# Kernel optimization log

Measured on AMD Instinct MI355X. Metric: run time of the kernel, lower is better.

Reference implementation:

```python
import jax, jax.numpy as jnp
import numpy as np
import math

NUM_HEADS = 16
HEAD_DIM = 32  # latent_dim // num_heads = 512 // 16


def rope(x, pos):
    # x: (B, H, S, Dh); half-split rotary embedding, theta=10000
    d = x.shape[-1] // 2
    inv_freq = 1.0 / (10000.0 ** (jnp.arange(d, dtype=jnp.float32) / d))
    ang = pos.astype(jnp.float32)[:, None] * inv_freq[None, :]  # (S, d)
    cos, sin = jnp.cos(ang), jnp.sin(ang)
    x1, x2 = x[..., :d], x[..., d:]
    return jnp.concatenate([x1 * cos - x2 * sin, x1 * sin + x2 * cos], axis=-1)


def setup_inputs() -> dict:
    key = jax.random.key(0)
    ks = jax.random.split(key, 16)
    B, L, KV_PREV = 1, 2048, 2048
    D, D_KV = 2048, 512
    s = lambda fan_in: 1.0 / math.sqrt(fan_in)
    return {
        "x": jax.random.normal(ks[0], (B, L, D), jnp.float32),
        "z_cache": jax.random.normal(ks[1], (B, KV_PREV, D_KV), jnp.float32),
        "valid_lens": jax.random.randint(ks[2], (B, L), 1, KV_PREV + L, jnp.int32),
        "W_latent": jax.random.normal(ks[3], (D, D_KV), jnp.float32) * s(D),
        "b_latent": jnp.zeros((D_KV,), jnp.float32),
        "W_q": jax.random.normal(ks[4], (D, NUM_HEADS * HEAD_DIM), jnp.float32) * s(D),
        "b_q": jnp.zeros((NUM_HEADS * HEAD_DIM,), jnp.float32),
        "W_k": jax.random.normal(ks[5], (D_KV, NUM_HEADS * HEAD_DIM), jnp.float32) * s(D_KV),
        "b_k": jnp.zeros((NUM_HEADS * HEAD_DIM,), jnp.float32),
        "W_v": jax.random.normal(ks[6], (D_KV, NUM_HEADS * HEAD_DIM), jnp.float32) * s(D_KV),
        "b_v": jnp.zeros((NUM_HEADS * HEAD_DIM,), jnp.float32),
        "W_o": jax.random.normal(ks[7], (NUM_HEADS * HEAD_DIM, D), jnp.float32) * s(NUM_HEADS * HEAD_DIM),
        "b_o": jnp.zeros((D,), jnp.float32),
    }


def reference(x, z_cache, valid_lens, W_latent, b_latent, W_q, b_q, W_k, b_k, W_v, b_v, W_o, b_o):
    B, L, D = x.shape
    H, Dh = NUM_HEADS, HEAD_DIM
    # latent projection + cache concat
    z_new = x @ W_latent + b_latent                      # (B, L, D_kv)
    z = jnp.concatenate([z_cache, z_new], axis=1)        # (B, KV, D_kv)
    KV = z.shape[1]
    q = (x @ W_q + b_q).reshape(B, L, H, Dh).transpose(0, 2, 1, 3)   # (B,H,L,Dh)
    k = (z @ W_k + b_k).reshape(B, KV, H, Dh).transpose(0, 2, 1, 3)  # (B,H,KV,Dh)
    v = (z @ W_v + b_v).reshape(B, KV, H, Dh).transpose(0, 2, 1, 3)  # (B,H,KV,Dh)
    q = rope(q, jnp.arange(L))
    k = rope(k, jnp.arange(KV))
    scores = jnp.einsum("bhqd,bhkd->bhqk", q, k) / math.sqrt(Dh)     # (B,H,L,KV)
    # faithful: unmasked softmax (returned as attn_weights), then re-masked softmax
    attn_weights = jax.nn.softmax(scores, axis=-1)
    invalid = jnp.arange(KV)[None, None, None, :] >= valid_lens[:, None, :, None]
    masked = jnp.where(invalid, jnp.float32(-10000.0), scores)
    masked_w = jax.nn.softmax(masked, axis=-1)
    heads = jnp.einsum("bhqk,bhkd->bhqd", masked_w, v)               # (B,H,L,Dh)
    heads = heads.transpose(0, 2, 1, 3).reshape(B, L, H * Dh)
    output = heads @ W_o + b_o                                       # (B, L, D)
    return (output, z, attn_weights, scores)
```

## Files before the change

### kernel.cpp

```cpp
#include <hip/hip_runtime.h>
#include <math.h>

#define L_Q     2048
#define KV_PREV 2048
#define KV_TOT  4096
#define DIM     2048
#define D_KV    512
#define NH      16
#define DH      32
#define HDh     512
#define KC      256

typedef short bf16x8 __attribute__((ext_vector_type(8)));
typedef short bf16x4 __attribute__((ext_vector_type(4)));
typedef float f32x4  __attribute__((ext_vector_type(4)));

__device__ inline short f2bf(float f) {
    unsigned u = __float_as_uint(f);
    u += 0x7fff + ((u >> 16) & 1);
    return (short)(u >> 16);
}

__device__ __constant__ double c_invfreq[16] = {
    1.0, 0.5623413251903491, 0.31622776601683794, 0.17782794100389228,
    0.1, 0.05623413251903491, 0.03162277660168379, 0.017782794100389228,
    0.01, 0.005623413251903491, 0.0031622776601683794, 0.0017782794100389228,
    0.001, 0.0005623413251903491, 0.00031622776601683794, 0.00017782794100389227,
};

__global__ void cvt_bf16(const float* __restrict__ in, short* __restrict__ out, int n8) {
    int i = blockIdx.x * blockDim.x + threadIdx.x;
    if (i >= n8) return;
    float4 a = reinterpret_cast<const float4*>(in)[2 * i];
    float4 b = reinterpret_cast<const float4*>(in)[2 * i + 1];
    union { short s[8]; int4 v; } u;
    u.s[0] = f2bf(a.x); u.s[1] = f2bf(a.y); u.s[2] = f2bf(a.z); u.s[3] = f2bf(a.w);
    u.s[4] = f2bf(b.x); u.s[5] = f2bf(b.y); u.s[6] = f2bf(b.z); u.s[7] = f2bf(b.w);
    reinterpret_cast<int4*>(out)[i] = u.v;
}

__global__ void cvt_copy(const float* __restrict__ src, float* __restrict__ dst,
                         short* __restrict__ dbf, int n8) {
    int i = blockIdx.x * blockDim.x + threadIdx.x;
    if (i >= n8) return;
    float4 a = reinterpret_cast<const float4*>(src)[2 * i];
    float4 b = reinterpret_cast<const float4*>(src)[2 * i + 1];
    reinterpret_cast<float4*>(dst)[2 * i]     = a;
    reinterpret_cast<float4*>(dst)[2 * i + 1] = b;
    union { short s[8]; int4 v; } u;
    u.s[0] = f2bf(a.x); u.s[1] = f2bf(a.y); u.s[2] = f2bf(a.z); u.s[3] = f2bf(a.w);
    u.s[4] = f2bf(b.x); u.s[5] = f2bf(b.y); u.s[6] = f2bf(b.z); u.s[7] = f2bf(b.w);
    reinterpret_cast<int4*>(dbf)[i] = u.v;
}

__global__ __launch_bounds__(256) void tr_cvt(const float* __restrict__ in,
        short* __restrict__ out, int K, int N) {
    __shared__ float tile[32][33];
    int k0 = blockIdx.x * 32, n0 = blockIdx.y * 32;
    int c = threadIdx.x & 31, r0 = threadIdx.x >> 5;
    for (int r = r0; r < 32; r += 8)
        tile[r][c] = in[(size_t)(k0 + r) * N + n0 + c];
    __syncthreads();
    for (int r = r0; r < 32; r += 8)
        out[(size_t)(n0 + r) * K + k0 + c] = f2bf(tile[c][r]);
}

__global__ __launch_bounds__(256) void vt_cvt(const short* __restrict__ v, short* __restrict__ vt) {
    __shared__ short tile[64][34];
    int h = blockIdx.y, kv0 = blockIdx.x * 64;
    int c = threadIdx.x & 31, r0 = threadIdx.x >> 5;
    for (int r = r0; r < 64; r += 8)
        tile[r][c] = v[(size_t)(kv0 + r) * HDh + h * DH + c];
    __syncthreads();
    int l = threadIdx.x & 63, wv = threadIdx.x >> 6;
    for (int d = wv; d < 32; d += 4)
        vt[((size_t)h * DH + d) * KV_TOT + kv0 + l] = tile[l][d];
}

__global__ __launch_bounds__(256) void gemm_bf16(const short* __restrict__ A,
        const short* __restrict__ Bt, const float* __restrict__ bias,
        float* __restrict__ C, short* __restrict__ Cbf, int rope,
        int M, int N, int K)
{
    int t = threadIdx.x, w = t >> 6, l = t & 63, lr = l & 15, lg = l >> 4;
    int m0 = blockIdx.y * 64 + w * 16;
    int n0 = blockIdx.x * 64;
    f32x4 acc[4] = {{0,0,0,0},{0,0,0,0},{0,0,0,0},{0,0,0,0}};
    const short* ap  = A  + (size_t)(m0 + lr) * K + lg * 8;
    const short* bp0 = Bt + (size_t)(n0 + lr) * K + lg * 8;
    #pragma unroll 2
    for (int k0 = 0; k0 < K; k0 += 32) {
        bf16x8 a = *reinterpret_cast<const bf16x8*>(ap + k0);
        #pragma unroll
        for (int j = 0; j < 4; ++j) {
            bf16x8 b = *reinterpret_cast<const bf16x8*>(bp0 + (size_t)j * 16 * K + k0);
            acc[j] = __builtin_amdgcn_mfma_f32_16x16x32_bf16(a, b, acc[j], 0, 0, 0);
        }
    }
    float bs[4];
    #pragma unroll
    for (int j = 0; j < 4; ++j) bs[j] = bias[n0 + j * 16 + lr];

    if (rope) {
        #pragma unroll
        for (int r = 0; r < 4; ++r) {
            int m = m0 + lg * 4 + r;
            float ang = (float)((double)m * c_invfreq[lr]);
            float cs = cosf(ang), sn = sinf(ang);
            size_t rb = (size_t)m * N + n0 + lr;
            float a1 = acc[0][r] + bs[0], a2 = acc[1][r] + bs[1];
            Cbf[rb]      = f2bf(a1 * cs - a2 * sn);
            Cbf[rb + 16] = f2bf(a1 * sn + a2 * cs);
            float b1 = acc[2][r] + bs[2], b2 = acc[3][r] + bs[3];
            Cbf[rb + 32] = f2bf(b1 * cs - b2 * sn);
            Cbf[rb + 48] = f2bf(b1 * sn + b2 * cs);
        }
        return;
    }
    #pragma unroll
    for (int j = 0; j < 4; ++j) {
        int n = n0 + j * 16 + lr;
        #pragma unroll
        for (int r = 0; r < 4; ++r) {
            float v = acc[j][r] + bs[j];
            size_t idx = (size_t)(m0 + lg * 4 + r) * N + n;
            if (C)   C[idx] = v;
            if (Cbf) Cbf[idx] = f2bf(v);
        }
    }
}

__global__ __launch_bounds__(256) void scores_stats(const short* __restrict__ q,
        const short* __restrict__ kmat, const int* __restrict__ vlens,
        float* __restrict__ scores, float* __restrict__ isu_o, float* __restrict__ is2_o)
{
    __shared__ float Sl[4][16][KC + 4];
    int t = threadIdx.x, w = t >> 6, l = t & 63, lr = l & 15, lg = l >> 4;
    int h = blockIdx.y;
    int qrow = blockIdx.x * 64 + w * 16;
    int myq = qrow + lr;
    bf16x8 bQ = *reinterpret_cast<const bf16x8*>(q + (size_t)myq * HDh + h * DH + lg * 8);
    int vl = vlens[myq];
    const short* kp = kmat + h * DH + lg * 8;
    const float sc = 0.17677669529663687f;
    float su = 0.f, s2 = 0.f;
    const int kb = lg * 4;

    bf16x8 a0 = *reinterpret_cast<const bf16x8*>(kp + (size_t)lr * HDh);
    bf16x8 a1 = *reinterpret_cast<const bf16x8*>(kp + (size_t)(16 + lr) * HDh);
    for (int c = 0; c < KV_TOT / KC; ++c) {
        #pragma unroll
        for (int kt = 0; kt < KC / 32; ++kt) {
            int k0 = c * KC + kt * 32;
            int kn = (k0 + 32) & (KV_TOT - 1);
            bf16x8 a0n = *reinterpret_cast<const bf16x8*>(kp + (size_t)(kn + lr) * HDh);
            bf16x8 a1n = *reinterpret_cast<const bf16x8*>(kp + (size_t)(kn + 16 + lr) * HDh);
            f32x4 z4 = {0.f, 0.f, 0.f, 0.f};
            f32x4 s0 = __builtin_amdgcn_mfma_f32_16x16x32_bf16(a0, bQ, z4, 0, 0, 0);
            f32x4 s1 = __builtin_amdgcn_mfma_f32_16x16x32_bf16(a1, bQ, z4, 0, 0, 0);
            f32x4 o0, o1;
            #pragma unroll
            for (int r = 0; r < 4; ++r) { o0[r] = s0[r] * sc; o1[r] = s1[r] * sc; }
            *reinterpret_cast<f32x4*>(&Sl[w][lr][kt * 32 + kb])      = o0;
            *reinterpret_cast<f32x4*>(&Sl[w][lr][kt * 32 + 16 + kb]) = o1;
            #pragma unroll
            for (int r = 0; r < 4; ++r) {
                float e0 = __expf(o0[r]), e1 = __expf(o1[r]);
                su += e0 + e1;
                if (k0 + kb + r < vl)      s2 += e0;
                if (k0 + 16 + kb + r < vl) s2 += e1;
            }
            a0 = a0n; a1 = a1n;
        }
        #pragma unroll
        for (int r = 0; r < 16; ++r) {
            f32x4 v = *reinterpret_cast<const f32x4*>(&Sl[w][r][l * 4]);
            float* dst = scores + ((size_t)h * L_Q + qrow + r) * KV_TOT + c * KC + l * 4;
            __builtin_nontemporal_store(v, reinterpret_cast<f32x4*>(dst));
        }
    }
    su += __shfl_xor(su, 16, 64); su += __shfl_xor(su, 32, 64);
    s2 += __shfl_xor(s2, 16, 64); s2 += __shfl_xor(s2, 32, 64);
    if (lg == 0) {
        size_t idx = (size_t)h * L_Q + myq;
        isu_o[idx] = 1.f / su;
        is2_o[idx] = 1.f / s2;
    }
}

__global__ __launch_bounds__(256) void attn_pv(const short* __restrict__ q,
        const short* __restrict__ kmat, const int* __restrict__ vlens,
        const float* __restrict__ isu_i, const float* __restrict__ is2_i,
        const short* __restrict__ Vt,
        float* __restrict__ attn, short* __restrict__ heads_bf)
{
    __shared__ float Al[4][16][KC + 4];
    __shared__ short Plds[4][16][72];
    int t = threadIdx.x, w = t >> 6, l = t & 63, lr = l & 15, lg = l >> 4;
    int h = blockIdx.y;
    int qrow = blockIdx.x * 64 + w * 16;
    int myq = qrow + lr;
    bf16x8 bQ = *reinterpret_cast<const bf16x8*>(q + (size_t)myq * HDh + h * DH + lg * 8);
    int vl = vlens[myq];
    size_t sidx = (size_t)h * L_Q + myq;
    float isu = isu_i[sidx], is2 = is2_i[sidx];
    const short* kp  = kmat + h * DH + lg * 8;
    const short* vp0 = Vt + ((size_t)h * DH + lr) * KV_TOT + lg * 8;
    const short* vp1 = vp0 + (size_t)16 * KV_TOT;
    const float sc = 0.17677669529663687f;
    short* prow = &Plds[w][lr][0];
    f32x4 h0 = {0,0,0,0}, h1 = {0,0,0,0};

    for (int c = 0; c < KV_TOT / KC; ++c) {
        #pragma unroll
        for (int g = 0; g < KC / 64; ++g) {
            #pragma unroll
            for (int kt = 0; kt < 4; ++kt) {
                int kk = c * KC + g * 64 + kt * 16;
                bf16x8 aK = *reinterpret_cast<const bf16x8*>(kp + (size_t)(kk + lr) * HDh);
                f32x4 z4 = {0.f, 0.f, 0.f, 0.f};
                f32x4 s = __builtin_amdgcn_mfma_f32_16x16x32_bf16(aK, bQ, z4, 0, 0, 0);
                f32x4 oa;
                bf16x4 pb;
                #pragma unroll
                for (int r = 0; r < 4; ++r) {
                    float e = __expf(s[r] * sc);
                    oa[r] = e * isu;
                    pb[r] = (kk + lg * 4 + r < vl) ? f2bf(e * is2) : (short)0;
                }
                *reinterpret_cast<f32x4*>(&Al[w][lr][g * 64 + kt * 16 + lg * 4]) = oa;
                *reinterpret_cast<bf16x4*>(prow + kt * 16 + lg * 4) = pb;
            }
            #pragma unroll
            for (int kbl = 0; kbl < 2; ++kbl) {
                int kv = c * KC + g * 64 + kbl * 32;
                bf16x8 pa = *reinterpret_cast<const bf16x8*>(prow + kbl * 32 + lg * 8);
                bf16x8 b0 = *reinterpret_cast<const bf16x8*>(vp0 + kv);
                bf16x8 b1 = *reinterpret_cast<const bf16x8*>(vp1 + kv);
                h0 = __builtin_amdgcn_mfma_f32_16x16x32_bf16(pa, b0, h0, 0, 0, 0);
                h1 = __builtin_amdgcn_mfma_f32_16x16x32_bf16(pa, b1, h1, 0, 0, 0);
            }
        }
        #pragma unroll
        for (int r = 0; r < 16; ++r) {
            f32x4 v = *reinterpret_cast<const f32x4*>(&Al[w][r][l * 4]);
            float* dst = attn + ((size_t)h * L_Q + qrow + r) * KV_TOT + c * KC + l * 4;
            __builtin_nontemporal_store(v, reinterpret_cast<f32x4*>(dst));
        }
    }
    #pragma unroll
    for (int r = 0; r < 4; ++r) {
        size_t ho = (size_t)(qrow + lg * 4 + r) * HDh + h * DH + lr;
        heads_bf[ho]      = f2bf(h0[r]);
        heads_bf[ho + 16] = f2bf(h1[r]);
    }
}

extern "C" void kernel_launch(void* const* d_in, const int* in_sizes, int n_in,
                              void* d_out, int out_size, void* d_ws, size_t ws_size,
                              hipStream_t stream) {
    const float* x       = (const float*)d_in[0];
    const float* z_cache = (const float*)d_in[1];
    const int*   vlens   = (const int*)  d_in[2];
    const float* W_lat   = (const float*)d_in[3];
    const float* b_lat   = (const float*)d_in[4];
    const float* W_q     = (const float*)d_in[5];
    const float* b_q     = (const float*)d_in[6];
    const float* W_k     = (const float*)d_in[7];
    const float* b_k     = (const float*)d_in[8];
    const float* W_v     = (const float*)d_in[9];
    const float* b_v     = (const float*)d_in[10];
    const float* W_o     = (const float*)d_in[11];
    const float* b_o     = (const float*)d_in[12];

    float* out        = (float*)d_out;
    float* out_output = out;
    float* out_z      = out_output + (size_t)L_Q * DIM;
    float* out_attn   = out_z + (size_t)KV_TOT * D_KV;
    float* out_scores = out_attn + (size_t)NH * L_Q * KV_TOT;

    float* wf     = (float*)d_ws;
    float* ws_isu = wf;
    float* ws_is2 = ws_isu + (size_t)NH * L_Q;
    short* wsb      = (short*)(ws_is2 + (size_t)NH * L_Q);
    short* x_bf     = wsb;
    short* z_bf     = x_bf + (size_t)L_Q * DIM;
    short* q_bf     = z_bf + (size_t)KV_TOT * D_KV;
    short* k_bf     = q_bf + (size_t)L_Q * HDh;
    short* v_bf     = k_bf + (size_t)KV_TOT * HDh;
    short* Vt       = v_bf + (size_t)KV_TOT * HDh;
    short* heads_bf = Vt + (size_t)NH * DH * KV_TOT;
    short* Wt_lat   = heads_bf + (size_t)L_Q * HDh;
    short* Wt_q     = Wt_lat + (size_t)D_KV * DIM;
    short* Wt_k     = Wt_q + (size_t)HDh * DIM;
    short* Wt_v     = Wt_k + (size_t)HDh * D_KV;
    short* Wt_o     = Wt_v + (size_t)HDh * D_KV;

    cvt_bf16<<<(L_Q * DIM / 8 + 255) / 256, 256, 0, stream>>>(x, x_bf, L_Q * DIM / 8);
    cvt_copy<<<(KV_PREV * D_KV / 8 + 255) / 256, 256, 0, stream>>>(
        z_cache, out_z, z_bf, KV_PREV * D_KV / 8);
    tr_cvt<<<dim3(DIM / 32, D_KV / 32), 256, 0, stream>>>(W_lat, Wt_lat, DIM, D_KV);
    tr_cvt<<<dim3(DIM / 32, HDh / 32), 256, 0, stream>>>(W_q, Wt_q, DIM, HDh);
    tr_cvt<<<dim3(D_KV / 32, HDh / 32), 256, 0, stream>>>(W_k, Wt_k, D_KV, HDh);
    tr_cvt<<<dim3(D_KV / 32, HDh / 32), 256, 0, stream>>>(W_v, Wt_v, D_KV, HDh);
    tr_cvt<<<dim3(HDh / 32, DIM / 32), 256, 0, stream>>>(W_o, Wt_o, HDh, DIM);

    gemm_bf16<<<dim3(D_KV / 64, L_Q / 64), 256, 0, stream>>>(
        x_bf, Wt_lat, b_lat, out_z + (size_t)KV_PREV * D_KV,
        z_bf + (size_t)KV_PREV * D_KV, 0, L_Q, D_KV, DIM);

    gemm_bf16<<<dim3(HDh / 64, L_Q / 64), 256, 0, stream>>>(
        x_bf, Wt_q, b_q, nullptr, q_bf, 1, L_Q, HDh, DIM);
    gemm_bf16<<<dim3(HDh / 64, KV_TOT / 64), 256, 0, stream>>>(
        z_bf, Wt_k, b_k, nullptr, k_bf, 1, KV_TOT, HDh, D_KV);
    gemm_bf16<<<dim3(HDh / 64, KV_TOT / 64), 256, 0, stream>>>(
        z_bf, Wt_v, b_v, nullptr, v_bf, 0, KV_TOT, HDh, D_KV);
    vt_cvt<<<dim3(KV_TOT / 64, NH), 256, 0, stream>>>(v_bf, Vt);

    scores_stats<<<dim3(L_Q / 64, NH), 256, 0, stream>>>(
        q_bf, k_bf, vlens, out_scores, ws_isu, ws_is2);

    attn_pv<<<dim3(L_Q / 64, NH), 256, 0, stream>>>(
        q_bf, k_bf, vlens, ws_isu, ws_is2, Vt, out_attn, heads_bf);

    gemm_bf16<<<dim3(DIM / 64, L_Q / 64), 256, 0, stream>>>(
        heads_bf, Wt_o, b_o, out_output, nullptr, 0, L_Q, DIM, HDh);
}
```

Baseline: 560.1 us.

## Prefetch whole K/V chunks into registers and shrink chunk size

New measurement: 586.1 us. 4.6% more time.

```diff
diff --git a/kernel.cpp b/kernel.cpp
--- a/kernel.cpp
+++ b/kernel.cpp
@@ -9,7 +9,7 @@
 #define NH      16
 #define DH      32
 #define HDh     512
-#define KC      256
+#define KC      128
 
 typedef short bf16x8 __attribute__((ext_vector_type(8)));
 typedef short bf16x4 __attribute__((ext_vector_type(4)));
@@ -146,38 +146,41 @@
     float su = 0.f, s2 = 0.f;
     const int kb = lg * 4;
 
-    bf16x8 a0 = *reinterpret_cast<const bf16x8*>(kp + (size_t)lr * HDh);
-    bf16x8 a1 = *reinterpret_cast<const bf16x8*>(kp + (size_t)(16 + lr) * HDh);
+    bf16x8 a[8], an[8];
+    #pragma unroll
+    for (int i = 0; i < 8; ++i)
+        a[i] = *reinterpret_cast<const bf16x8*>(kp + (size_t)(i * 16 + lr) * HDh);
+
+    #pragma unroll 2
     for (int c = 0; c < KV_TOT / KC; ++c) {
-        #pragma unroll
-        for (int kt = 0; kt < KC / 32; ++kt) {
-            int k0 = c * KC + kt * 32;
-            int kn = (k0 + 32) & (KV_TOT - 1);
-            bf16x8 a0n = *reinterpret_cast<const bf16x8*>(kp + (size_t)(kn + lr) * HDh);
-            bf16x8 a1n = *reinterpret_cast<const bf16x8*>(kp + (size_t)(kn + 16 + lr) * HDh);
+        int kbase = c * KC;
+        int knext = (kbase + KC) & (KV_TOT - 1);
+        #pragma unroll
+        for (int i = 0; i < 8; ++i)
+            an[i] = *reinterpret_cast<const bf16x8*>(kp + (size_t)(knext + i * 16 + lr) * HDh);
+        #pragma unroll
+        for (int i = 0; i < 8; ++i) {
             f32x4 z4 = {0.f, 0.f, 0.f, 0.f};
-            f32x4 s0 = __builtin_amdgcn_mfma_f32_16x16x32_bf16(a0, bQ, z4, 0, 0, 0);
-            f32x4 s1 = __builtin_amdgcn_mfma_f32_16x16x32_bf16(a1, bQ, z4, 0, 0, 0);
-            f32x4 o0, o1;
-            #pragma unroll
-            for (int r = 0; r < 4; ++r) { o0[r] = s0[r] * sc; o1[r] = s1[r] * sc; }
-            *reinterpret_cast<f32x4*>(&Sl[w][lr][kt * 32 + kb])      = o0;
-            *reinterpret_cast<f32x4*>(&Sl[w][lr][kt * 32 + 16 + kb]) = o1;
+            f32x4 s = __builtin_amdgcn_mfma_f32_16x16x32_bf16(a[i], bQ, z4, 0, 0, 0);
+            f32x4 o;
+            #pragma unroll
+            for (int r = 0; r < 4; ++r) o[r] = s[r] * sc;
+            *reinterpret_cast<f32x4*>(&Sl[w][lr][i * 16 + kb]) = o;
             #pragma unroll
             for (int r = 0; r < 4; ++r) {
-                float e0 = __expf(o0[r]), e1 = __expf(o1[r]);
-                su += e0 + e1;
-                if (k0 + kb + r < vl)      s2 += e0;
-                if (k0 + 16 + kb + r < vl) s2 += e1;
+                float e = __expf(o[r]);
+                su += e;
+                if (kbase + i * 16 + kb + r < vl) s2 += e;
             }
-            a0 = a0n; a1 = a1n;
         }
         #pragma unroll
         for (int r = 0; r < 16; ++r) {
-            f32x4 v = *reinterpret_cast<const f32x4*>(&Sl[w][r][l * 4]);
-            float* dst = scores + ((size_t)h * L_Q + qrow + r) * KV_TOT + c * KC + l * 4;
-            __builtin_nontemporal_store(v, reinterpret_cast<f32x4*>(dst));
-        }
+            float2 v = *reinterpret_cast<const float2*>(&Sl[w][r][l * 2]);
+            *reinterpret_cast<float2*>(
+                scores + ((size_t)h * L_Q + qrow + r) * KV_TOT + kbase + l * 2) = v;
+        }
+        #pragma unroll
+        for (int i = 0; i < 8; ++i) a[i] = an[i];
     }
     su += __shfl_xor(su, 16, 64); su += __shfl_xor(su, 32, 64);
     s2 += __shfl_xor(s2, 16, 64); s2 += __shfl_xor(s2, 32, 64);
@@ -208,45 +211,71 @@
     const short* vp0 = Vt + ((size_t)h * DH + lr) * KV_TOT + lg * 8;
     const short* vp1 = vp0 + (size_t)16 * KV_TOT;
     const float sc = 0.17677669529663687f;
+    const int kb = lg * 4;
     short* prow = &Plds[w][lr][0];
     f32x4 h0 = {0,0,0,0}, h1 = {0,0,0,0};
 
+    bf16x8 aK[8], aKn[8], vf[8], vfn[8];
+    #pragma unroll
+    for (int i = 0; i < 8; ++i)
+        aK[i] = *reinterpret_cast<const bf16x8*>(kp + (size_t)(i * 16 + lr) * HDh);
+    #pragma unroll
+    for (int g = 0; g < 2; ++g)
+        #pragma unroll
+        for (int kbl = 0; kbl < 2; ++kbl) {
+            vf[g * 4 + kbl * 2 + 0] = *reinterpret_cast<const bf16x8*>(vp0 + g * 64 + kbl * 32);
+            vf[g * 4 + kbl * 2 + 1] = *reinterpret_cast<const bf16x8*>(vp1 + g * 64 + kbl * 32);
+        }
+
+    #pragma unroll 2
     for (int c = 0; c < KV_TOT / KC; ++c) {
-        #pragma unroll
-        for (int g = 0; g < KC / 64; ++g) {
+        int kbase = c * KC;
+        int knext = (kbase + KC) & (KV_TOT - 1);
+        #pragma unroll
+        for (int i = 0; i < 8; ++i)
+            aKn[i] = *reinterpret_cast<const bf16x8*>(kp + (size_t)(knext + i * 16 + lr) * HDh);
+        #pragma unroll
+        for (int g = 0; g < 2; ++g)
+            #pragma unroll
+            for (int kbl = 0; kbl < 2; ++kbl) {
+                vfn[g * 4 + kbl * 2 + 0] =
+                    *reinterpret_cast<const bf16x8*>(vp0 + knext + g * 64 + kbl * 32);
+                vfn[g * 4 + kbl * 2 + 1] =
+                    *reinterpret_cast<const bf16x8*>(vp1 + knext + g * 64 + kbl * 32);
+            }
+        #pragma unroll
+        for (int g = 0; g < 2; ++g) {
             #pragma unroll
             for (int kt = 0; kt < 4; ++kt) {
-                int kk = c * KC + g * 64 + kt * 16;
-                bf16x8 aK = *reinterpret_cast<const bf16x8*>(kp + (size_t)(kk + lr) * HDh);
+                int i = g * 4 + kt;
                 f32x4 z4 = {0.f, 0.f, 0.f, 0.f};
-                f32x4 s = __builtin_amdgcn_mfma_f32_16x16x32_bf16(aK, bQ, z4, 0, 0, 0);
+                f32x4 s = __builtin_amdgcn_mfma_f32_16x16x32_bf16(aK[i], bQ, z4, 0, 0, 0);
                 f32x4 oa;
                 bf16x4 pb;
                 #pragma unroll
                 for (int r = 0; r < 4; ++r) {
                     float e = __expf(s[r] * sc);
                     oa[r] = e * isu;
-                    pb[r] = (kk + lg * 4 + r < vl) ? f2bf(e * is2) : (short)0;
+                    pb[r] = (kbase + i * 16 + kb + r < vl) ? f2bf(e * is2) : (short)0;
                 }
-                *reinterpret_cast<f32x4*>(&Al[w][lr][g * 64 + kt * 16 + lg * 4]) = oa;
-                *reinterpret_cast<bf16x4*>(prow + kt * 16 + lg * 4) = pb;
+                *reinterpret_cast<f32x4*>(&Al[w][lr][i * 16 + kb]) = oa;
+                *reinterpret_cast<bf16x4*>(prow + kt * 16 + kb) = pb;
             }
             #pragma unroll
             for (int kbl = 0; kbl < 2; ++kbl) {
-                int kv = c * KC + g * 64 + kbl * 32;
                 bf16x8 pa = *reinterpret_cast<const bf16x8*>(prow + kbl * 32 + lg * 8);
-                bf16x8 b0 = *reinterpret_cast<const bf16x8*>(vp0 + kv);
-                bf16x8 b1 = *reinterpret_cast<const bf16x8*>(vp1 + kv);
-                h0 = __builtin_amdgcn_mfma_f32_16x16x32_bf16(pa, b0, h0, 0, 0, 0);
-                h1 = __builtin_amdgcn_mfma_f32_16x16x32_bf16(pa, b1, h1, 0, 0, 0);
+                h0 = __builtin_amdgcn_mfma_f32_16x16x32_bf16(pa, vf[g * 4 + kbl * 2 + 0], h0, 0, 0, 0);
+                h1 = __builtin_amdgcn_mfma_f32_16x16x32_bf16(pa, vf[g * 4 + kbl * 2 + 1], h1, 0, 0, 0);
             }
         }
         #pragma unroll
         for (int r = 0; r < 16; ++r) {
-            f32x4 v = *reinterpret_cast<const f32x4*>(&Al[w][r][l * 4]);
-            float* dst = attn + ((size_t)h * L_Q + qrow + r) * KV_TOT + c * KC + l * 4;
-            __builtin_nontemporal_store(v, reinterpret_cast<f32x4*>(dst));
-        }
+            float2 v = *reinterpret_cast<const float2*>(&Al[w][r][l * 2]);
+            *reinterpret_cast<float2*>(
+                attn + ((size_t)h * L_Q + qrow + r) * KV_TOT + kbase + l * 2) = v;
+        }
+        #pragma unroll
+        for (int i = 0; i < 8; ++i) { aK[i] = aKn[i]; vf[i] = vfn[i]; }
     }
     #pragma unroll
     for (int r = 0; r < 4; ++r) {
```

## Split KV range across warps in score and attention kernels

Applied to the files above, without the earlier changes.

New measurement: 556.7 us. Within noise of the previous version (-0.6%).

```diff
diff --git a/kernel.cpp b/kernel.cpp
--- a/kernel.cpp
+++ b/kernel.cpp
@@ -10,6 +10,7 @@
 #define DH      32
 #define HDh     512
 #define KC      256
+#define KQ      (KV_TOT / 4)
 
 typedef short bf16x8 __attribute__((ext_vector_type(8)));
 typedef short bf16x4 __attribute__((ext_vector_type(4)));
@@ -135,9 +136,10 @@
         float* __restrict__ scores, float* __restrict__ isu_o, float* __restrict__ is2_o)
 {
     __shared__ float Sl[4][16][KC + 4];
+    __shared__ float red[4][16][2];
     int t = threadIdx.x, w = t >> 6, l = t & 63, lr = l & 15, lg = l >> 4;
     int h = blockIdx.y;
-    int qrow = blockIdx.x * 64 + w * 16;
+    int qrow = blockIdx.x * 16;
     int myq = qrow + lr;
     bf16x8 bQ = *reinterpret_cast<const bf16x8*>(q + (size_t)myq * HDh + h * DH + lg * 8);
     int vl = vlens[myq];
@@ -145,14 +147,16 @@
     const float sc = 0.17677669529663687f;
     float su = 0.f, s2 = 0.f;
     const int kb = lg * 4;
-
-    bf16x8 a0 = *reinterpret_cast<const bf16x8*>(kp + (size_t)lr * HDh);
-    bf16x8 a1 = *reinterpret_cast<const bf16x8*>(kp + (size_t)(16 + lr) * HDh);
-    for (int c = 0; c < KV_TOT / KC; ++c) {
+    const int kq0 = w * KQ;
+
+    bf16x8 a0 = *reinterpret_cast<const bf16x8*>(kp + (size_t)(kq0 + lr) * HDh);
+    bf16x8 a1 = *reinterpret_cast<const bf16x8*>(kp + (size_t)(kq0 + 16 + lr) * HDh);
+    for (int c = 0; c < KQ / KC; ++c) {
+        int kbase = kq0 + c * KC;
         #pragma unroll
         for (int kt = 0; kt < KC / 32; ++kt) {
-            int k0 = c * KC + kt * 32;
-            int kn = (k0 + 32) & (KV_TOT - 1);
+            int k0 = kbase + kt * 32;
+            int kn = kq0 + ((c * KC + kt * 32 + 32) & (KQ - 1));
             bf16x8 a0n = *reinterpret_cast<const bf16x8*>(kp + (size_t)(kn + lr) * HDh);
             bf16x8 a1n = *reinterpret_cast<const bf16x8*>(kp + (size_t)(kn + 16 + lr) * HDh);
             f32x4 z4 = {0.f, 0.f, 0.f, 0.f};
@@ -172,19 +176,24 @@
             }
             a0 = a0n; a1 = a1n;
         }
+        __builtin_amdgcn_s_barrier();
         #pragma unroll
         for (int r = 0; r < 16; ++r) {
             f32x4 v = *reinterpret_cast<const f32x4*>(&Sl[w][r][l * 4]);
-            float* dst = scores + ((size_t)h * L_Q + qrow + r) * KV_TOT + c * KC + l * 4;
-            __builtin_nontemporal_store(v, reinterpret_cast<f32x4*>(dst));
+            __builtin_nontemporal_store(v, reinterpret_cast<f32x4*>(
+                scores + ((size_t)h * L_Q + qrow + r) * KV_TOT + kbase + l * 4));
         }
     }
     su += __shfl_xor(su, 16, 64); su += __shfl_xor(su, 32, 64);
     s2 += __shfl_xor(s2, 16, 64); s2 += __shfl_xor(s2, 32, 64);
-    if (lg == 0) {
-        size_t idx = (size_t)h * L_Q + myq;
-        isu_o[idx] = 1.f / su;
-        is2_o[idx] = 1.f / s2;
+    if (lg == 0) { red[w][lr][0] = su; red[w][lr][1] = s2; }
+    __syncthreads();
+    if (t < 16) {
+        float sut = red[0][t][0] + red[1][t][0] + red[2][t][0] + red[3][t][0];
+        float s2t = red[0][t][1] + red[1][t][1] + red[2][t][1] + red[3][t][1];
+        size_t idx = (size_t)h * L_Q + qrow + t;
+        isu_o[idx] = 1.f / sut;
+        is2_o[idx] = 1.f / s2t;
     }
 }
 
@@ -198,7 +207,7 @@
     __shared__ short Plds[4][16][72];
     int t = threadIdx.x, w = t >> 6, l = t & 63, lr = l & 15, lg = l >> 4;
     int h = blockIdx.y;
-    int qrow = blockIdx.x * 64 + w * 16;
+    int qrow = blockIdx.x * 16;
     int myq = qrow + lr;
     bf16x8 bQ = *reinterpret_cast<const bf16x8*>(q + (size_t)myq * HDh + h * DH + lg * 8);
     int vl = vlens[myq];
@@ -208,16 +217,20 @@
     const short* vp0 = Vt + ((size_t)h * DH + lr) * KV_TOT + lg * 8;
     const short* vp1 = vp0 + (size_t)16 * KV_TOT;
     const float sc = 0.17677669529663687f;
+    const int kb = lg * 4;
+    const int kq0 = w * KQ;
     short* prow = &Plds[w][lr][0];
     f32x4 h0 = {0,0,0,0}, h1 = {0,0,0,0};
 
-    for (int c = 0; c < KV_TOT / KC; ++c) {
-        #pragma unroll
-        for (int g = 0; g < KC / 64; ++g) {
+    for (int c = 0; c < KQ / KC; ++c) {
+        int kbase = kq0 + c * KC;
+        #pragma unroll
+        for (int g = 0; g < 4; ++g) {
             #pragma unroll
             for (int kt = 0; kt < 4; ++kt) {
-                int kk = c * KC + g * 64 + kt * 16;
-                bf16x8 aK = *reinterpret_cast<const bf16x8*>(kp + (size_t)(kk + lr) * HDh);
+                int i = g * 4 + kt;
+                bf16x8 aK = *reinterpret_cast<const bf16x8*>(
+                    kp + (size_t)(kbase + i * 16 + lr) * HDh);
                 f32x4 z4 = {0.f, 0.f, 0.f, 0.f};
                 f32x4 s = __builtin_amdgcn_mfma_f32_16x16x32_bf16(aK, bQ, z4, 0, 0, 0);
                 f32x4 oa;
@@ -226,14 +239,14 @@
                 for (int r = 0; r < 4; ++r) {
                     float e = __expf(s[r] * sc);
                     oa[r] = e * isu;
-                    pb[r] = (kk + lg * 4 + r < vl) ? f2bf(e * is2) : (short)0;
+                    pb[r] = (kbase + i * 16 + kb + r < vl) ? f2bf(e * is2) : (short)0;
                 }
-                *reinterpret_cast<f32x4*>(&Al[w][lr][g * 64 + kt * 16 + lg * 4]) = oa;
-                *reinterpret_cast<bf16x4*>(prow + kt * 16 + lg * 4) = pb;
+                *reinterpret_cast<f32x4*>(&Al[w][lr][i * 16 + kb]) = oa;
+                *reinterpret_cast<bf16x4*>(prow + kt * 16 + kb) = pb;
             }
             #pragma unroll
             for (int kbl = 0; kbl < 2; ++kbl) {
-                int kv = c * KC + g * 64 + kbl * 32;
+                int kv = kbase + g * 64 + kbl * 32;
                 bf16x8 pa = *reinterpret_cast<const bf16x8*>(prow + kbl * 32 + lg * 8);
                 bf16x8 b0 = *reinterpret_cast<const bf16x8*>(vp0 + kv);
                 bf16x8 b1 = *reinterpret_cast<const bf16x8*>(vp1 + kv);
@@ -241,18 +254,34 @@
                 h1 = __builtin_amdgcn_mfma_f32_16x16x32_bf16(pa, b1, h1, 0, 0, 0);
             }
         }
+        __builtin_amdgcn_s_barrier();
         #pragma unroll
         for (int r = 0; r < 16; ++r) {
             f32x4 v = *reinterpret_cast<const f32x4*>(&Al[w][r][l * 4]);
-            float* dst = attn + ((size_t)h * L_Q + qrow + r) * KV_TOT + c * KC + l * 4;
-            __builtin_nontemporal_store(v, reinterpret_cast<f32x4*>(dst));
-        }
-    }
-    #pragma unroll
-    for (int r = 0; r < 4; ++r) {
-        size_t ho = (size_t)(qrow + lg * 4 + r) * HDh + h * DH + lr;
-        heads_bf[ho]      = f2bf(h0[r]);
-        heads_bf[ho + 16] = f2bf(h1[r]);
+            __builtin_nontemporal_store(v, reinterpret_cast<f32x4*>(
+                attn + ((size_t)h * L_Q + qrow + r) * KV_TOT + kbase + l * 4));
+        }
+    }
+    __syncthreads();
+    float* hst = &Al[0][0][0];
+    if (w > 0) {
+        *reinterpret_cast<f32x4*>(&hst[((w - 1) * 64 + l) * 8])     = h0;
+        *reinterpret_cast<f32x4*>(&hst[((w - 1) * 64 + l) * 8 + 4]) = h1;
+    }
+    __syncthreads();
+    if (w == 0) {
+        #pragma unroll
+        for (int ww = 0; ww < 3; ++ww) {
+            f32x4 g0 = *reinterpret_cast<const f32x4*>(&hst[(ww * 64 + l) * 8]);
+            f32x4 g1 = *reinterpret_cast<const f32x4*>(&hst[(ww * 64 + l) * 8 + 4]);
+            h0 += g0; h1 += g1;
+        }
+        #pragma unroll
+        for (int r = 0; r < 4; ++r) {
+            size_t ho = (size_t)(qrow + lg * 4 + r) * HDh + h * DH + lr;
+            heads_bf[ho]      = f2bf(h0[r]);
+            heads_bf[ho + 16] = f2bf(h1[r]);
+        }
     }
 }
 
@@ -317,10 +346,10 @@
         z_bf, Wt_v, b_v, nullptr, v_bf, 0, KV_TOT, HDh, D_KV);
     vt_cvt<<<dim3(KV_TOT / 64, NH), 256, 0, stream>>>(v_bf, Vt);
 
-    scores_stats<<<dim3(L_Q / 64, NH), 256, 0, stream>>>(
+    scores_stats<<<dim3(L_Q / 16, NH), 256, 0, stream>>>(
         q_bf, k_bf, vlens, out_scores, ws_isu, ws_is2);
 
-    attn_pv<<<dim3(L_Q / 64, NH), 256, 0, stream>>>(
+    attn_pv<<<dim3(L_Q / 16, NH), 256, 0, stream>>>(
         q_bf, k_bf, vlens, ws_isu, ws_is2, Vt, out_attn, heads_bf);
 
     gemm_bf16<<<dim3(DIM / 64, L_Q / 64), 256, 0, stream>>>(
```
